# Kernel tuning notes

Measured on AMD Instinct MI355X. Metric: run time of the kernel, lower is better.

## Reference

```python
import jax, jax.numpy as jnp
import numpy as np

EPS = 1e-8
CG_TOL = 1e-4
S_SIGMA = 8   # bilateral grid spatial downsampling
N_BINS = 9    # bilateral grid range bins (intensity in [0,1])


def _conv2d(x, k):
    # x [C,H,W], k [kh,kw] -> same-padded cross-correlation, per channel
    kh, kw = k.shape
    out = jax.lax.conv_general_dilated(x[:, None], k[None, None], (1, 1),
                                       [(kh // 2, kh // 2), (kw // 2, kw // 2)])
    return out[:, 0]


def _conv2d_T(x, k):
    return _conv2d(x, k[::-1, ::-1])


def _conv_bank(x, ks):
    # x [C,H,W], ks [N,kh,kw] -> [N,C,H,W]
    n, kh, kw = ks.shape
    out = jax.lax.conv_general_dilated(x[:, None], ks[:, None], (1, 1),
                                       [(kh // 2, kh // 2), (kw // 2, kw // 2)])
    return out.transpose(1, 0, 2, 3)


def _conv_bank_T(v, ks):
    # v [N,C,H,W] -> sum_n conv(v[n], flip(ks[n])) : [C,H,W]
    n, kh, kw = ks.shape
    lhs = v.transpose(1, 0, 2, 3)          # [C,N,H,W]
    rhs = ks[:, ::-1, ::-1][None]          # [1,N,kh,kw]
    out = jax.lax.conv_general_dilated(lhs, rhs, (1, 1),
                                       [(kh // 2, kh // 2), (kw // 2, kw // 2)])
    return out[:, 0]


def _deconv_grad(blurred, x, kernel, dkw, dks, rkw, rks, rpow, reg_targets):
    # gradient of E(x) = sum_i dkw_i ||dk_i * (k*x - b)||^2
    #                  + sum_j rkw_j sum |rk_j*x - t_j|^{p_j}
    Kx = _conv2d(x, kernel) - blurred
    d = _conv_bank(Kx, dks)                                    # [Nd,C,H,W]
    g = _conv2d_T(_conv_bank_T(2.0 * dkw[:, None, None, None] * d, dks), kernel)
    v = _conv_bank(x, rks) - reg_targets                       # [Nr,C,H,W]
    av = jnp.abs(v) + EPS
    phi = jnp.sign(v) * av ** (rpow[:, None, None, None] - 1.0)
    g = g + _conv_bank_T(rkw[:, None, None, None] * rpow[:, None, None, None] * phi, rks)
    return g


def _deconv_alpha(blurred, x, kernel, dkw, dks, rkw, rks, rpow, reg_targets, p):
    # exact line search for the quadratic part, Gauss-Newton for |.|^p prior
    g = _deconv_grad(blurred, x, kernel, dkw, dks, rkw, rks, rpow, reg_targets)
    num = -jnp.sum(g * p)
    Kp = _conv2d(p, kernel)
    dKp = _conv_bank(Kp, dks)
    den = jnp.sum(2.0 * dkw[:, None, None, None] * dKp ** 2)
    v = _conv_bank(x, rks) - reg_targets
    Rp = _conv_bank(p, rks)
    w = (rkw * rpow * (rpow - 1.0))[:, None, None, None]
    den = den + jnp.sum(w * (jnp.abs(v) + EPS) ** (rpow[:, None, None, None] - 2.0) * Rp ** 2)
    return num / (den + 1e-12)


def _deconv_prior(x, rks, thr):
    # soft-shrinkage of filtered responses -> regularization targets
    v = _conv_bank(x, rks)
    return jnp.sign(v) * jnp.maximum(jnp.abs(v) - thr[:, None, None, None], 0.0)


def _conv_axis(g, f, axis):
    k = f.shape[0]; r = k // 2; L = g.shape[axis]
    pad = [(0, 0)] * g.ndim; pad[axis] = (r, r)
    gp = jnp.pad(g, pad)
    out = jnp.zeros_like(g)
    for t in range(k):  # fixed small tap count
        out = out + f[t] * jax.lax.slice_in_dim(gp, t, t + L, axis=axis)
    return out


def _bilateral_channel(I, fs, fr):
    # learned-filter bilateral grid: splat -> separable filter (fs,fs,fr) -> trilinear slice
    H, W = I.shape
    gh, gw = H // S_SIGMA, W // S_SIGMA
    Ic = jnp.clip(I, 0.0, 1.0)
    yy, xx = jnp.meshgrid(jnp.arange(H), jnp.arange(W), indexing="ij")
    yi = yy // S_SIGMA; xi = xx // S_SIGMA
    zi = jnp.clip(jnp.round(Ic * (N_BINS - 1)).astype(jnp.int32), 0, N_BINS - 1)
    flat = ((yi * gw + xi) * N_BINS + zi).ravel()
    gv = jnp.zeros(gh * gw * N_BINS, Ic.dtype).at[flat].add(Ic.ravel())
    gw_ = jnp.zeros(gh * gw * N_BINS, Ic.dtype).at[flat].add(1.0)
    g2 = jnp.stack([gv, gw_], -1).reshape(gh, gw, N_BINS, 2)
    g2 = _conv_axis(_conv_axis(_conv_axis(g2, fs, 0), fs, 1), fr, 2)
    yf = yy / S_SIGMA; xf = xx / S_SIGMA; zf = Ic * (N_BINS - 1)

    def corners(f, n):
        c0 = jnp.clip(jnp.floor(f).astype(jnp.int32), 0, n - 1)
        c1 = jnp.minimum(c0 + 1, n - 1)
        w = jnp.clip(f - c0, 0.0, 1.0)
        return c0, c1, w

    y0, y1, wy = corners(yf, gh)
    x0, x1, wx = corners(xf, gw)
    z0, z1, wz = corners(zf, N_BINS)
    acc = jnp.zeros(I.shape + (2,), Ic.dtype)
    for yc, wyc in ((y0, 1 - wy), (y1, wy)):
        for xc, wxc in ((x0, 1 - wx), (x1, wx)):
            for zc, wzc in ((z0, 1 - wz), (z1, wz)):
                acc = acc + (wyc * wxc * wzc)[..., None] * g2[yc, xc, zc]
    return acc[..., 0] / (acc[..., 1] + 1e-8)


def _forward(blurred_batch, kernel_batch, data_kernels, data_kernel_weights,
             reg_kernels, reg_kernel_weights, reg_powers, filter_s, filter_r,
             reg_thresholds, num_cg_iter):
    num_stages = filter_s.shape[0]
    n_reg = reg_kernels.shape[1]

    def single(blurred, kernel):
        def cg(x, idx, reg_targets):
            dkw = data_kernel_weights[idx]; dks = data_kernels[idx]
            rkw = reg_kernel_weights[idx]; rks = reg_kernels[idx]; rp = reg_powers[idx]
            g = _deconv_grad(blurred, x, kernel, dkw, dks, rkw, rks, rp, reg_targets)
            r = -g
            r_norm = jnp.sum(r * r)
            r0 = r_norm

            def body(i, carry):
                x, r, p, rn, done = carry
                alpha = _deconv_alpha(blurred, x, kernel, dkw, dks, rkw, rks, rp, reg_targets, p)
                x1 = x + alpha * p
                g1 = _deconv_grad(blurred, x1, kernel, dkw, dks, rkw, rks, rp, reg_targets)
                r1 = -g1
                nrn = jnp.sum(r1 * r1)
                beta = nrn / (rn + 1e-20)
                conv_now = nrn < CG_TOL * r0
                p1 = r1 + beta * p
                x_n = jnp.where(done, x, x1)
                r_n = jnp.where(done, r, r1)
                rn_n = jnp.where(done, rn, nrn)
                p_n = jnp.where(done | conv_now, p, p1)
                return (x_n, r_n, p_n, rn_n, done | conv_now)

            carry = (x, r, r, r_norm, jnp.array(False))
            x, _, _, _, _ = jax.lax.fori_loop(0, num_cg_iter, body, carry)
            return x

        x = cg(blurred, 0, jnp.zeros((n_reg,) + blurred.shape, blurred.dtype))
        for stage in range(num_stages):
            x = jax.vmap(lambda ch: _bilateral_channel(ch, filter_s[stage], filter_r[stage]))(x)
            reg_targets = _deconv_prior(x, reg_kernels[stage + 1], reg_thresholds[stage])
            x = cg(x, stage + 1, reg_targets)
        return x

    return jax.vmap(single)(blurred_batch, kernel_batch)


def setup_inputs() -> dict:
    key = jax.random.key(0)
    k1, k2 = jax.random.split(key)
    B, C, H, W, KS = 2, 3, 512, 512, 15
    blurred = jax.random.uniform(k1, (B, C, H, W), jnp.float32)
    kern = jax.random.uniform(k2, (B, KS, KS), jnp.float32)
    kern = kern / jnp.sum(kern, axis=(1, 2), keepdims=True)  # normalized PSFs

    ns = 1; c = 2  # num_stages, kernel center (5x5)
    rk = np.zeros((ns + 1, 5, 5, 5), np.float32)
    rk[:, 0, c, c] = -1.0; rk[:, 0, c + 1, c] = 1.0
    rk[:, 1, c, c] = -1.0; rk[:, 1, c, c + 1] = 1.0
    rk[:, 2, c, c] = 1.0; rk[:, 2, c + 1, c] = -1.0
    rk[:, 2, c, c + 1] = -1.0; rk[:, 2, c + 1, c + 1] = 1.0
    rk[:, 3, c - 1, c] = 1.0; rk[:, 3, c, c] = -2.0; rk[:, 3, c + 1, c] = 1.0
    rk[:, 4, c, c - 1] = 1.0; rk[:, 4, c, c] = -2.0; rk[:, 4, c, c + 1] = 1.0
    dk = np.zeros((ns + 1, 6, 5, 5), np.float32)
    dk[:, 0, c, c] = 1.0
    dk[:, 1:] = rk
    dkw = np.zeros((ns + 1, 6), np.float32); dkw[:, 0] = 1.0
    rkw = np.zeros((ns + 1, 5), np.float32)
    rkw[0, :] = 0.001; rkw[1:, :] = 0.05
    rpow = np.full((ns + 1, 5), 2.0, np.float32)
    fs = np.zeros((ns, 11), np.float32); fs[:, 3:8] = [0.0, 1.0, 2.0, 1.0, 0.0]
    fr = np.tile(np.array([0.0, 1.0, 2.0, 1.0, 0.0], np.float32), (ns, 1))
    thr = np.tile(np.array([0.065, 0.065, 0.0325, 0.0325, 0.0325], np.float32), (ns, 1))

    return {
        "blurred_batch": blurred,
        "kernel_batch": kern,
        "data_kernels": jnp.asarray(dk),
        "data_kernel_weights": jnp.asarray(dkw),
        "reg_kernels": jnp.asarray(rk),
        "reg_kernel_weights": jnp.asarray(rkw),
        "reg_powers": jnp.asarray(rpow),
        "filter_s": jnp.asarray(fs),
        "filter_r": jnp.asarray(fr),
        "reg_thresholds": jnp.asarray(thr),
        "num_cg_iter": 5,
    }


def reference(blurred_batch, kernel_batch, data_kernels, data_kernel_weights,
              reg_kernels, reg_kernel_weights, reg_powers, filter_s, filter_r,
              reg_thresholds, num_cg_iter):
    return _forward(blurred_batch, kernel_batch, data_kernels, data_kernel_weights,
                    reg_kernels, reg_kernel_weights, reg_powers, filter_s, filter_r,
                    reg_thresholds, num_cg_iter)
```

## Files before the change

### kernel.cpp

```cpp
#include <hip/hip_runtime.h>

constexpr int Bn = 2, Cn = 3, Hh = 512, Ww = 512;
constexpr int KS = 15, KR = 7;
constexpr int NDK = 6, NRK = 5;
constexpr int GH = 64, GW = 64, NBn = 9, SS = 8;
constexpr float EPSf = 1e-8f;
constexpr float CGTOL = 1e-4f;
constexpr int PLANE = Hh * Ww;
constexpr int CHW = Cn * PLANE;
constexpr int BX = 64, BY = 16;
constexpr int GXc = Ww / BX, GYc = Hh / BY;
constexpr int PB = GXc * GYc * Cn;
constexpr int SA = 80, THt = 30;
constexpr int S2W = 72, S2H = 24;
constexpr int PHW = 68, PHH = 20;
constexpr int PHG = (PHW / 4) * PHH;
constexpr int NITER = 5;

struct CgState { float alpha, beta, rn, r0; int done, pflag; int pad0, pad1; };

struct SolveInfo {
    int fastBank;
    int allrp2;
    int nd;
    int pad;
    float sctot;
    float dsc[NDK];
    int ddy[NDK], ddx[NDK];
    float C[81];
};

__device__ __forceinline__ float blockReduce(float v, float* red, int tid) {
    red[tid] = v; __syncthreads();
    for (int s = 128; s > 0; s >>= 1) { if (tid < s) red[tid] += red[tid + s]; __syncthreads(); }
    float r = red[0]; __syncthreads();
    return r;
}

__global__ __launch_bounds__(128)
void k_comp(const float* __restrict__ dkw, const float* __restrict__ dks,
            const float* __restrict__ rkw, const float* __restrict__ rpw,
            const float* __restrict__ rks, SolveInfo* si)
{
    const int idx = blockIdx.x;
    SolveInfo* s = si + idx;
    const float* dkw_i = dkw + idx * NDK;
    const float* dks_i = dks + (size_t)idx * NDK * 25;
    const float* rkw_i = rkw + idx * NRK;
    const float* rpw_i = rpw + idx * NRK;
    const float* rks_i = rks + (size_t)idx * NRK * 25;
    const int t = threadIdx.x;
    if (t < 81) {
        int oy = t / 9 - 4, ox = t % 9 - 4;
        float acc = 0.f;
        for (int m = 0; m < NRK; m++) {
            float wm = rkw_i[m], rp = rpw_i[m];
            float ch = wm * rp * (rp - 1.f);
            if (ch == 0.f) continue;
            for (int ay = 0; ay < 5; ay++)
                for (int ax = 0; ax < 5; ax++) {
                    int by = ay - oy, bx = ax - ox;
                    if (by < 0 || by >= 5 || bx < 0 || bx >= 5) continue;
                    acc += ch * rks_i[m * 25 + ay * 5 + ax] * rks_i[m * 25 + by * 5 + bx];
                }
        }
        s->C[t] = acc;
    }
    if (t == 81) {
        int fast = 1, nd = 0; float tot = 0.f;
        for (int n = 0; n < NDK; n++) {
            if (dkw_i[n] == 0.f) continue;
            int cntz = 0, pos = -1;
            for (int q = 0; q < 25; q++) if (dks_i[n * 25 + q] != 0.f) { cntz++; pos = q; }
            if (cntz > 1) fast = 0;
            if (cntz == 1 && nd < NDK) {
                float v = dks_i[n * 25 + pos];
                s->dsc[nd] = 2.f * dkw_i[n] * v * v;
                s->ddy[nd] = pos / 5 - 2; s->ddx[nd] = pos % 5 - 2;
                tot += s->dsc[nd]; nd++;
            }
        }
        s->fastBank = fast; s->nd = fast ? nd : 0; s->sctot = tot;
    }
    if (t == 82) {
        int ok = 1;
        for (int m = 0; m < NRK; m++) {
            float wm = rkw_i[m], rp = rpw_i[m];
            if (wm != 0.f && rp != 2.f && wm * rp * (rp - 1.f) != 0.f) ok = 0;
        }
        s->allrp2 = ok;
    }
}

__global__ __launch_bounds__(256)
void k_conv15(const float* __restrict__ src, const float* __restrict__ rb,
              const float* __restrict__ pbuf, float* __restrict__ aux2,
              const float* __restrict__ sub, float* __restrict__ out,
              const float* __restrict__ kernB, float* __restrict__ part,
              const SolveInfo* __restrict__ si,
              const CgState* __restrict__ st, const int* __restrict__ ncg,
              int iter, int mode)
{
    const int pz = blockIdx.z, b = pz / Cn, c = pz % Cn;
    const CgState s = st[b];
    if (mode == 2 && (s.done != 0 || iter >= *ncg)) return;
    __shared__ __align__(16) float tile[SA * THt];
    __shared__ float red[256];
    const int tx = threadIdx.x, ty = threadIdx.y, tid = ty * 16 + tx;
    const int ox0 = blockIdx.x * BX, oy0 = blockIdx.y * BY;
    const int baseP = pz * PLANE;
    const float beta = s.beta; const int pf = s.pflag;
// ... 88 lines not shown
    __shared__ __align__(16) float sl[S2W * S2H];
    __shared__ __align__(16) float dl[PHW * PHH];
    __shared__ float dkk[NDK * 25];
    __shared__ float dww[NDK];
    const int tx = threadIdx.x, ty = threadIdx.y, tid = ty * 16 + tx;
    const int ox0 = blockIdx.x * BX, oy0 = blockIdx.y * BY;
    const int baseP = pz * PLANE;
    const int colbase = tx * 4;
    for (int i = tid; i < NDK * 25; i += 256) dkk[i] = dks[i];
    if (tid < NDK) dww[tid] = dkw[tid];
    for (int i = tid; i < S2W * S2H; i += 256) {
        int ly = i / S2W, lx = i % S2W;
        int gy = oy0 - 4 + ly, gx = ox0 - 4 + lx;
        sl[i] = (gy >= 0 && gy < Hh && gx >= 0 && gx < Ww) ? sbuf[baseP + gy * Ww + gx] : 0.f;
    }
    __syncthreads();
    float t0 = 0.f, t1 = 0.f, t2 = 0.f, t3 = 0.f;
    for (int n = 0; n < NDK; n++) {
        float wn = 2.f * dww[n];
        if (wn == 0.f) continue;
        float dnr[25];
        #pragma unroll
        for (int q = 0; q < 25; q++) dnr[q] = dkk[n * 25 + q];
        for (int t = tid; t < PHG; t += 256) {
            int zy = t / 17, zx0 = (t % 17) * 4;
            int gy = oy0 - 2 + zy, gx0 = ox0 - 2 + zx0;
            float v0 = 0.f, v1 = 0.f, v2 = 0.f, v3 = 0.f;
            #pragma unroll
            for (int a = 0; a < 5; a++) {
                bool rz = dnr[a*5]==0.f && dnr[a*5+1]==0.f && dnr[a*5+2]==0.f &&
                          dnr[a*5+3]==0.f && dnr[a*5+4]==0.f;
                if (rz) continue;
                const float4* s4 = reinterpret_cast<const float4*>(&sl[(zy + a) * S2W + zx0]);
                float4 u0 = s4[0], u1 = s4[1];
                float f8[8] = {u0.x,u0.y,u0.z,u0.w,u1.x,u1.y,u1.z,u1.w};
                #pragma unroll
                for (int bb = 0; bb < 5; bb++) {
                    float kv = dnr[a * 5 + bb];
                    if (kv != 0.f) {
                        v0 = fmaf(kv, f8[bb], v0); v1 = fmaf(kv, f8[bb+1], v1);
                        v2 = fmaf(kv, f8[bb+2], v2); v3 = fmaf(kv, f8[bb+3], v3);
                    }
                }
            }
            bool gyin = (gy >= 0 && gy < Hh);
            if (!gyin || gx0     < 0 || gx0     >= Ww) v0 = 0.f;
            if (!gyin || gx0 + 1 < 0 || gx0 + 1 >= Ww) v1 = 0.f;
            if (!gyin || gx0 + 2 < 0 || gx0 + 2 >= Ww) v2 = 0.f;
            if (!gyin || gx0 + 3 < 0 || gx0 + 3 >= Ww) v3 = 0.f;
            *reinterpret_cast<float4*>(&dl[zy * PHW + zx0]) = make_float4(v0, v1, v2, v3);
        }
        __syncthreads();
        float c0 = 0.f, c1 = 0.f, c2 = 0.f, c3 = 0.f;
        #pragma unroll
        for (int a = 0; a < 5; a++) {
            int fr = 4 - a;
            bool rz = dnr[fr*5]==0.f && dnr[fr*5+1]==0.f && dnr[fr*5+2]==0.f &&
                      dnr[fr*5+3]==0.f && dnr[fr*5+4]==0.f;
            if (rz) continue;
            const float4* q4 = reinterpret_cast<const float4*>(&dl[(ty + a) * PHW + colbase]);
            float4 u0 = q4[0], u1 = q4[1];
            float f8[8] = {u0.x,u0.y,u0.z,u0.w,u1.x,u1.y,u1.z,u1.w};
            #pragma unroll
            for (int bb = 0; bb < 5; bb++) {
                float kv = dnr[fr * 5 + (4 - bb)];
                if (kv != 0.f) {
                    c0 = fmaf(kv, f8[bb], c0); c1 = fmaf(kv, f8[bb+1], c1);
                    c2 = fmaf(kv, f8[bb+2], c2); c3 = fmaf(kv, f8[bb+3], c3);
                }
            }
        }
        t0 = fmaf(wn, c0, t0); t1 = fmaf(wn, c1, t1);
        t2 = fmaf(wn, c2, t2); t3 = fmaf(wn, c3, t3);
        __syncthreads();
    }
    const int gi = baseP + (oy0 + ty) * Ww + ox0 + colbase;
    *reinterpret_cast<float4*>(&tbuf[gi]) = make_float4(t0, t1, t2, t3);
}

__global__ __launch_bounds__(256)
void k_hess(const float* __restrict__ kx, const float* __restrict__ wb,
            const float* __restrict__ pn,
            float* __restrict__ qb, const float* __restrict__ kernB,
            const float* __restrict__ rks, const float* __restrict__ rkw,
            const float* __restrict__ rpw, const SolveInfo* __restrict__ si,
            float* __restrict__ part, const CgState* __restrict__ st,
            const int* __restrict__ ncg, int iter)
{
    if (!si->allrp2) return;
    const int pz = blockIdx.z, b = pz / Cn, c = pz % Cn;
    const CgState s = st[b];
    if (s.done != 0 || iter >= *ncg) return;
    __shared__ __align__(16) float wt[SA * THt];
    __shared__ __align__(16) float s2[S2W * S2H];
    __shared__ __align__(16) float sC[81];
    __shared__ float rk5[NRK * 25];
    __shared__ float srkw[NRK], srpw[NRK];
    __shared__ float red[256];
    float* ph = wt;
    const int tx = threadIdx.x, ty = threadIdx.y, tid = ty * 16 + tx;
    const int ox0 = blockIdx.x * BX, oy0 = blockIdx.y * BY;
    const int baseP = pz * PLANE;
    const float* wsrc = si->fastBank ? kx : wb;
    const float* kp = kernB + b * 225;

    for (int i = tid; i < 81; i += 256) sC[i] = si->C[i];
    for (int i = tid; i < NRK * 25; i += 256) rk5[i] = rks[i];
    if (tid < NRK) { srkw[tid] = rkw[tid]; srpw[tid] = rpw[tid]; }

    for (int i = tid; i < 78 * THt; i += 256) {
        int ly = i / 78, lx = i % 78;
        int gy = oy0 - KR + ly, gx = ox0 - KR + lx;
        wt[ly * SA + lx] = (gy >= 0 && gy < Hh && gx >= 0 && gx < Ww)
                           ? wsrc[baseP + gy * Ww + gx] : 0.f;
    }
    for (int i = tid; i < S2W * S2H; i += 256) {
        int ly = i / S2W, lx = i % S2W;
        int gy = oy0 - 4 + ly, gx = ox0 - 4 + lx;
        s2[i] = (gy >= 0 && gy < Hh && gx >= 0 && gx < Ww)
                ? pn[baseP + gy * Ww + gx] : 0.f;
    }
    __syncthreads();

    const int colbase = tx * 4;
    float a0 = 0.f, a1 = 0.f, a2 = 0.f, a3 = 0.f;
    for (int i = 0; i < KS; i++) {
        const float4* rp4 = reinterpret_cast<const float4*>(&wt[(ty + i) * SA + colbase]);
        float f[20];
        #pragma unroll
        for (int s5 = 0; s5 < 5; s5++) {
            float4 w4 = rp4[s5];
            f[s5 * 4] = w4.x; f[s5 * 4 + 1] = w4.y; f[s5 * 4 + 2] = w4.z; f[s5 * 4 + 3] = w4.w;
        }
        const float* kr = kp + (14 - i) * 15;
        #pragma unroll
        for (int j = 0; j < KS; j++) {
            float kv = kr[14 - j];
            a0 = fmaf(kv, f[j], a0); a1 = fmaf(kv, f[j + 1], a1);
            a2 = fmaf(kv, f[j + 2], a2); a3 = fmaf(kv, f[j + 3], a3);
        }
    }

    const bool blkInterior = (oy0 >= 2) && (oy0 + BY - 1 <= Hh - 3) &&
                             (ox0 >= 2) && (ox0 + BX - 1 <= Ww - 3);
    if (blkInterior) {
        #pragma unroll
        for (int oy = 0; oy < 9; oy++) {
            float cr[9]; bool nz = false;
            #pragma unroll
            for (int ox = 0; ox < 9; ox++) { cr[ox] = sC[oy * 9 + ox]; nz = nz || (cr[ox] != 0.f); }
            if (!nz) continue;
            const float4* s4 = reinterpret_cast<const float4*>(&s2[(ty + oy) * S2W + colbase]);
            float4 u0 = s4[0], u1 = s4[1], u2 = s4[2];
            float f12[12] = {u0.x,u0.y,u0.z,u0.w,u1.x,u1.y,u1.z,u1.w,u2.x,u2.y,u2.z,u2.w};
            #pragma unroll
            for (int ox = 0; ox < 9; ox++) {
                float kv = cr[ox];
                if (kv != 0.f) {
                    a0 = fmaf(kv, f12[ox], a0); a1 = fmaf(kv, f12[ox + 1], a1);
                    a2 = fmaf(kv, f12[ox + 2], a2); a3 = fmaf(kv, f12[ox + 3], a3);
                }
            }
        }
    } else {
        __syncthreads();
        for (int m = 0; m < NRK; m++) {
            float wm = srkw[m], rp = srpw[m];
            float coefH = wm * rp * (rp - 1.f);
            if (coefH == 0.f) continue;
            float rmr[25];
            #pragma unroll
            for (int q = 0; q < 25; q++) rmr[q] = rk5[m * 25 + q];
            for (int t = tid; t < PHG; t += 256) {
                int zy = t / 17, zx0 = (t % 17) * 4;
                int gy = oy0 - 2 + zy, gx0 = ox0 - 2 + zx0;
                float v0 = 0.f, v1 = 0.f, v2 = 0.f, v3 = 0.f;
                #pragma unroll
                for (int a = 0; a < 5; a++) {
                    bool rz = rmr[a*5]==0.f && rmr[a*5+1]==0.f && rmr[a*5+2]==0.f &&
                              rmr[a*5+3]==0.f && rmr[a*5+4]==0.f;
                    if (rz) continue;
                    const float4* s4 = reinterpret_cast<const float4*>(&s2[(zy + a) * S2W + zx0]);
                    float4 u0 = s4[0], u1 = s4[1];
                    float f8[8] = {u0.x,u0.y,u0.z,u0.w,u1.x,u1.y,u1.z,u1.w};
                    #pragma unroll
                    for (int bb = 0; bb < 5; bb++) {
                        float kv = rmr[a * 5 + bb];
                        if (kv != 0.f) {
                            v0 = fmaf(kv, f8[bb], v0); v1 = fmaf(kv, f8[bb+1], v1);
                            v2 = fmaf(kv, f8[bb+2], v2); v3 = fmaf(kv, f8[bb+3], v3);
                        }
                    }
                }
                bool gyin = (gy >= 0 && gy < Hh);
                if (!gyin || gx0     < 0 || gx0     >= Ww) v0 = 0.f;
                if (!gyin || gx0 + 1 < 0 || gx0 + 1 >= Ww) v1 = 0.f;
                if (!gyin || gx0 + 2 < 0 || gx0 + 2 >= Ww) v2 = 0.f;
                if (!gyin || gx0 + 3 < 0 || gx0 + 3 >= Ww) v3 = 0.f;
                *reinterpret_cast<float4*>(&ph[zy * PHW + zx0]) =
                    make_float4(coefH * v0, coefH * v1, coefH * v2, coefH * v3);
            }
            __syncthreads();
            #pragma unroll
            for (int a = 0; a < 5; a++) {
                int fr = 4 - a;
                bool rz = rmr[fr*5]==0.f && rmr[fr*5+1]==0.f && rmr[fr*5+2]==0.f &&
                          rmr[fr*5+3]==0.f && rmr[fr*5+4]==0.f;
                if (rz) continue;
                const float4* q4 = reinterpret_cast<const float4*>(&ph[(ty + a) * PHW + colbase]);
                float4 u0 = q4[0], u1 = q4[1];
                float f8[8] = {u0.x,u0.y,u0.z,u0.w,u1.x,u1.y,u1.z,u1.w};
                #pragma unroll
                for (int bb = 0; bb < 5; bb++) {
                    float kv = rmr[fr * 5 + (4 - bb)];
                    if (kv != 0.f) {
                        a0 = fmaf(kv, f8[bb], a0); a1 = fmaf(kv, f8[bb+1], a1);
                        a2 = fmaf(kv, f8[bb+2], a2); a3 = fmaf(kv, f8[bb+3], a3);
                    }
                }
            }
            __syncthreads();
        }
    }

    const int gy = oy0 + ty, gx0 = ox0 + colbase;
    const int gi = baseP + gy * Ww + gx0;
    *reinterpret_cast<float4*>(&qb[gi]) = make_float4(a0, a1, a2, a3);
    int li = (ty + 4) * S2W + colbase + 4;
    float redv = s2[li] * a0 + s2[li + 1] * a1 + s2[li + 2] * a2 + s2[li + 3] * a3;
    float tot = blockReduce(redv, red, tid);
    if (tid == 0) {
        int blk = c * (GXc * GYc) + blockIdx.y * GXc + blockIdx.x;
        part[((size_t)b * 4 + 1) * PB + blk] = tot;
    }
}

__global__ __launch_bounds__(256)
void k_gradL(const float* __restrict__ kx, const float* __restrict__ wb,
             const float* __restrict__ xg,
             const float* __restrict__ rb, const float* __restrict__ pbuf,
             const float* __restrict__ tgt, const float* __restrict__ thr,
             float* __restrict__ outb,
             float* __restrict__ pout, const float* __restrict__ kernB,
             const float* __restrict__ rks, const float* __restrict__ rkw,
             const float* __restrict__ rpw, const SolveInfo* __restrict__ si,
             float* __restrict__ part, const CgState* __restrict__ st,
             const int* __restrict__ ncg, int iter, int mode)
{
    if (mode == 1 && si->allrp2) return;
    const int pz = blockIdx.z, b = pz / Cn, c = pz % Cn;
    const CgState s = st[b];
    if (mode == 1 && (s.done != 0 || iter >= *ncg)) return;
    __shared__ __align__(16) float wt[SA * THt];
    __shared__ __align__(16) float s2[S2W * S2H];
    __shared__ __align__(16) float sC[81];
    __shared__ float rk5[NRK * 25];
    __shared__ float srkw[NRK], srpw[NRK], sthr[NRK];
    __shared__ float red[256];
    float* ph = wt;
    const int tx = threadIdx.x, ty = threadIdx.y, tid = ty * 16 + tx;
    const int ox0 = blockIdx.x * BX, oy0 = blockIdx.y * BY;
    const int baseP = pz * PLANE;
    const float beta = s.beta; const int pf = s.pflag;
    const float* wsrc = si->fastBank ? kx : wb;
    const float* kp = kernB + b * 225;

    for (int i = tid; i < 81; i += 256) sC[i] = si->C[i];
    for (int i = tid; i < NRK * 25; i += 256) rk5[i] = rks[i];
    if (tid < NRK) {
        srkw[tid] = rkw[tid]; srpw[tid] = rpw[tid];
        sthr[tid] = thr ? thr[tid] : 0.f;
    }

    for (int i = tid; i < 78 * THt; i += 256) {
        int ly = i / 78, lx = i % 78;
        int gy = oy0 - KR + ly, gx = ox0 - KR + lx;
        wt[ly * SA + lx] = (gy >= 0 && gy < Hh && gx >= 0 && gx < Ww)
                           ? wsrc[baseP + gy * Ww + gx] : 0.f;
    }
    for (int i = tid; i < S2W * S2H; i += 256) {
        int ly = i / S2W, lx = i % S2W;
        int gy = oy0 - 4 + ly, gx = ox0 - 4 + lx;
        float v = 0.f;
        if (gy >= 0 && gy < Hh && gx >= 0 && gx < Ww) {
            int gi = baseP + gy * Ww + gx;
            if (mode == 0) v = xg[gi];
            else { float rv = rb[gi], pv = pbuf[gi]; v = pf ? fmaf(beta, pv, rv) : pv; }
        }
        s2[i] = v;
    }
    __syncthreads();

    const int colbase = tx * 4;
    float a0 = 0.f, a1 = 0.f, a2 = 0.f, a3 = 0.f;
    for (int i = 0; i < KS; i++) {
        const float4* rp4 = reinterpret_cast<const float4*>(&wt[(ty + i) * SA + colbase]);
        float f[20];
        #pragma unroll
        for (int s5 = 0; s5 < 5; s5++) {
            float4 w4 = rp4[s5];
            f[s5 * 4] = w4.x; f[s5 * 4 + 1] = w4.y; f[s5 * 4 + 2] = w4.z; f[s5 * 4 + 3] = w4.w;
        }
        const float* kr = kp + (14 - i) * 15;
        #pragma unroll
        for (int j = 0; j < KS; j++) {
            float kv = kr[14 - j];
            a0 = fmaf(kv, f[j], a0); a1 = fmaf(kv, f[j + 1], a1);
            a2 = fmaf(kv, f[j + 2], a2); a3 = fmaf(kv, f[j + 3], a3);
        }
    }

    const bool blkInterior = (oy0 >= 2) && (oy0 + BY - 1 <= Hh - 3) &&
                             (ox0 >= 2) && (ox0 + BX - 1 <= Ww - 3);
    if (mode == 0 && si->allrp2 && thr == nullptr && blkInterior) {
        #pragma unroll
        for (int oy = 0; oy < 9; oy++) {
            float cr[9]; bool nz = false;
            #pragma unroll
            for (int ox = 0; ox < 9; ox++) { cr[ox] = sC[oy * 9 + ox]; nz = nz || (cr[ox] != 0.f); }
            if (!nz) continue;
            const float4* s4 = reinterpret_cast<const float4*>(&s2[(ty + oy) * S2W + colbase]);
            float4 u0 = s4[0], u1 = s4[1], u2 = s4[2];
            float f12[12] = {u0.x,u0.y,u0.z,u0.w,u1.x,u1.y,u1.z,u1.w,u2.x,u2.y,u2.z,u2.w};
            #pragma unroll
            for (int ox = 0; ox < 9; ox++) {
                float kv = cr[ox];
                if (kv != 0.f) {
                    a0 = fmaf(kv, f12[ox], a0); a1 = fmaf(kv, f12[ox + 1], a1);
                    a2 = fmaf(kv, f12[ox + 2], a2); a3 = fmaf(kv, f12[ox + 3], a3);
                }
            }
        }
    } else {
        __syncthreads();
        for (int m = 0; m < NRK; m++) {
            float wm = srkw[m], rp = srpw[m];
            if (wm == 0.f) continue;
            float rmr[25];
            #pragma unroll
            for (int q = 0; q < 25; q++) rmr[q] = rk5[m * 25 + q];
            const float* tgm = (mode == 1 && tgt)
                ? tgt + ((size_t)(b * NRK + m)) * CHW + (size_t)c * PLANE : nullptr;
            const float coefG = wm * rp;
            const float coefH = wm * rp * (rp - 1.f);
            const float thrm = sthr[m];

            for (int t = tid; t < PHG; t += 256) {
                int zy = t / 17, zx0 = (t % 17) * 4;
                int gy = oy0 - 2 + zy, gx0 = ox0 - 2 + zx0;
                float v0 = 0.f, v1 = 0.f, v2 = 0.f, v3 = 0.f;
                #pragma unroll
                for (int a = 0; a < 5; a++) {
                    bool rz = rmr[a*5]==0.f && rmr[a*5+1]==0.f && rmr[a*5+2]==0.f &&
                              rmr[a*5+3]==0.f && rmr[a*5+4]==0.f;
                    if (rz) continue;
                    const float4* s4 = reinterpret_cast<const float4*>(&s2[(zy + a) * S2W + zx0]);
                    float4 u0 = s4[0], u1 = s4[1];
                    float f8[8] = {u0.x,u0.y,u0.z,u0.w,u1.x,u1.y,u1.z,u1.w};
                    #pragma unroll
                    for (int bb = 0; bb < 5; bb++) {
                        float kv = rmr[a * 5 + bb];
                        if (kv != 0.f) {
                            v0 = fmaf(kv, f8[bb], v0); v1 = fmaf(kv, f8[bb+1], v1);
                            v2 = fmaf(kv, f8[bb+2], v2); v3 = fmaf(kv, f8[bb+3], v3);
                        }
                    }
                }
                bool gyin = (gy >= 0 && gy < Hh);
                float o0 = 0.f, o1 = 0.f, o2 = 0.f, o3 = 0.f;
                #pragma unroll
                for (int j = 0; j < 4; j++) {
                    int gx = gx0 + j;
                    if (!gyin || gx < 0 || gx >= Ww) continue;
                    float v = (j == 0) ? v0 : (j == 1) ? v1 : (j == 2) ? v2 : v3;
                    float o;
                    if (mode == 0) {
                        if (thr) {
                            float sgv = (v > 0.f) ? 1.f : ((v < 0.f) ? -1.f : 0.f);
                            v = sgv * fminf(fabsf(v), thrm);
                        }
                        float sg = (v > 0.f) ? 1.f : ((v < 0.f) ? -1.f : 0.f);
                        float av = fabsf(v) + EPSf;
                        o = coefG * sg * ((rp == 2.f) ? av : powf(av, rp - 1.f));
                    } else {
                        float fac = 1.f;
                        if (rp != 2.f) {
                            float vx = 0.f;
                            for (int a = 0; a < 5; a++)
                                for (int bb = 0; bb < 5; bb++) {
                                    int yy = gy - 2 + a, xx = gx - 2 + bb;
                                    if (yy >= 0 && yy < Hh && xx >= 0 && xx < Ww)
                                        vx = fmaf(rmr[a * 5 + bb], xg[baseP + yy * Ww + xx], vx);
                                }
                            if (tgm) vx -= tgm[gy * Ww + gx];
                            fac = powf(fabsf(vx) + EPSf, rp - 2.f);
                        }
                        o = coefH * fac * v;
                    }
                    if (j == 0) o0 = o; else if (j == 1) o1 = o; else if (j == 2) o2 = o; else o3 = o;
                }
                *reinterpret_cast<float4*>(&ph[zy * PHW + zx0]) = make_float4(o0, o1, o2, o3);
            }
            __syncthreads();
            #pragma unroll
            for (int a = 0; a < 5; a++) {
                int fr = 4 - a;
                bool rz = rmr[fr*5]==0.f && rmr[fr*5+1]==0.f && rmr[fr*5+2]==0.f &&
                          rmr[fr*5+3]==0.f && rmr[fr*5+4]==0.f;
                if (rz) continue;
                const float4* q4 = reinterpret_cast<const float4*>(&ph[(ty + a) * PHW + colbase]);
                float4 u0 = q4[0], u1 = q4[1];
                float f8[8] = {u0.x,u0.y,u0.z,u0.w,u1.x,u1.y,u1.z,u1.w};
                #pragma unroll
                for (int bb = 0; bb < 5; bb++) {
                    float kv = rmr[fr * 5 + (4 - bb)];
                    if (kv != 0.f) {
                        a0 = fmaf(kv, f8[bb], a0); a1 = fmaf(kv, f8[bb+1], a1);
                        a2 = fmaf(kv, f8[bb+2], a2); a3 = fmaf(kv, f8[bb+3], a3);
                    }
                }
            }
            __syncthreads();
        }
    }

    const int gi = baseP + (oy0 + ty) * Ww + ox0 + colbase;
    float redv;
    if (mode == 0) {
        float r0v = -a0, r1v = -a1, r2v = -a2, r3v = -a3;
        float4 rv4 = make_float4(r0v, r1v, r2v, r3v);
        *reinterpret_cast<float4*>(&outb[gi]) = rv4;
        *reinterpret_cast<float4*>(&pout[gi]) = rv4;
        redv = r0v * r0v + r1v * r1v + r2v * r2v + r3v * r3v;
    } else {
        *reinterpret_cast<float4*>(&outb[gi]) = make_float4(a0, a1, a2, a3);
        int li = (ty + 4) * S2W + colbase + 4;
        redv = s2[li] * a0 + s2[li + 1] * a1 + s2[li + 2] * a2 + s2[li + 3] * a3;
    }
    float tot = blockReduce(redv, red, tid);
    if (tid == 0) {
        int blk = c * (GXc * GYc) + blockIdx.y * GXc + blockIdx.x;
        int slot = (mode == 0) ? 2 : 1;
        part[((size_t)b * 4 + slot) * PB + blk] = tot;
    }
}

__global__ __launch_bounds__(256)
void k_axpy(float4* __restrict__ x, float4* __restrict__ r,
            const float4* __restrict__ pn, const float4* __restrict__ q,
            float* __restrict__ part, const CgState* __restrict__ st,
            const int* __restrict__ ncg, int iter)
{
    const int b = blockIdx.y;
    const CgState s = st[b];
    if (s.done != 0 || iter >= *ncg) return;
    __shared__ float red[256];
    const int tid = threadIdx.x;
    float sn = 0.f, sd = 0.f;
    for (int i = tid; i < PB; i += 256) {
        sn += part[((size_t)b * 4 + 0) * PB + i];
        sd += part[((size_t)b * 4 + 1) * PB + i];
    }
    float num = blockReduce(sn, red, tid);
    float den = blockReduce(sd, red, tid);
    const float alpha = num / (den + 1e-12f);
    const int idx = b * (CHW / 4) + blockIdx.x * 256 + tid;
    float4 pc = pn[idx], rv = r[idx], qv = q[idx], xv = x[idx];
    xv.x = fmaf(alpha, pc.x, xv.x); xv.y = fmaf(alpha, pc.y, xv.y);
    xv.z = fmaf(alpha, pc.z, xv.z); xv.w = fmaf(alpha, pc.w, xv.w);
    rv.x = fmaf(-alpha, qv.x, rv.x); rv.y = fmaf(-alpha, qv.y, rv.y);
    rv.z = fmaf(-alpha, qv.z, rv.z); rv.w = fmaf(-alpha, qv.w, rv.w);
    x[idx] = xv; r[idx] = rv;
    float nr = rv.x * rv.x + rv.y * rv.y + rv.z * rv.z + rv.w * rv.w;
    float tot = blockReduce(nr, red, tid);
    if (tid == 0) part[((size_t)b * 4 + 2) * PB + blockIdx.x] = tot;
}

__global__ __launch_bounds__(256)
void k_fin_iter(const float* __restrict__ part, CgState* st,
                const int* __restrict__ ncg, int iter, int mode)
{
    const int b = blockIdx.x, tid = threadIdx.x;
    __shared__ float red[256];
    if (mode == 1 && (st[b].done != 0 || iter >= *ncg)) { if (tid == 0) st[b].pflag = 0; return; }
    float s = 0.f;
    for (int i = tid; i < PB; i += 256) s += part[((size_t)b * 4 + 2) * PB + i];
    float nrn = blockReduce(s, red, tid);
    if (tid == 0) {
        if (mode == 0) {
            st[b].rn = nrn; st[b].r0 = nrn; st[b].done = 0; st[b].pflag = 0;
            st[b].beta = 0.f; st[b].alpha = 0.f;
        } else {
            float beta = nrn / (st[b].rn + 1e-20f);
            int conv = (nrn < CGTOL * st[b].r0) ? 1 : 0;
            st[b].beta = beta; st[b].rn = nrn;
            st[b].pflag = conv ? 0 : 1;
            if (conv) st[b].done = 1;
        }
    }
}

__global__ __launch_bounds__(64)
void k_splat(const float* __restrict__ x, float* __restrict__ grid)
{
    __shared__ float bins[NBn * 2];
    const int tid = threadIdx.y * 8 + threadIdx.x;
    if (tid < NBn * 2) bins[tid] = 0.f;
    __syncthreads();
    const int pz = blockIdx.z;
    const int gy = blockIdx.y, gx = blockIdx.x;
    const int py = gy * 8 + threadIdx.y, px = gx * 8 + threadIdx.x;
    float I = x[(size_t)pz * PLANE + py * Ww + px];
    float Ic = fminf(fmaxf(I, 0.f), 1.f);
    int zi = (int)rintf(Ic * (NBn - 1));
    zi = min(max(zi, 0), NBn - 1);
    atomicAdd(&bins[zi * 2], Ic);
    atomicAdd(&bins[zi * 2 + 1], 1.f);
    __syncthreads();
    if (tid < NBn * 2)
        grid[(size_t)pz * GH * GW * NBn * 2 + ((size_t)gy * GW + gx) * NBn * 2 + tid] = bins[tid];
}

__global__ __launch_bounds__(256)
void k_blur(const float* __restrict__ in, float* __restrict__ out,
            const float* __restrict__ taps, int ntaps, int axis)
{
    const int id = blockIdx.x * 256 + threadIdx.x;
    const int total = Bn * Cn * GH * GW * NBn;
    if (id >= total) return;
    const int z = id % NBn;
    const int x = (id / NBn) % GW;
    const int y = (id / (NBn * GW)) % GH;
    const int p = id / (NBn * GW * GH);
    int coord, lim; long stride;
    if (axis == 0)      { coord = y; lim = GH;  stride = (long)GW * NBn * 2; }
    else if (axis == 1) { coord = x; lim = GW;  stride = NBn * 2; }
    else                { coord = z; lim = NBn; stride = 2; }
    const long base = (((long)(p * GH + y) * GW + x) * NBn + z) * 2;
    const int r = ntaps / 2;
    float a0 = 0.f, a1 = 0.f;
    for (int t = 0; t < ntaps; t++) {
        int cc = coord + t - r;
        if (cc < 0 || cc >= lim) continue;
        float w = taps[t];
        long ofs = base + (long)(cc - coord) * stride;
        a0 = fmaf(w, in[ofs], a0);
        a1 = fmaf(w, in[ofs + 1], a1);
    }
    out[base] = a0; out[base + 1] = a1;
}

__global__ __launch_bounds__(256)
void k_slice(const float* __restrict__ xin, const float* __restrict__ grid,
             float* __restrict__ xout)
{
    const int pz = blockIdx.z;
    const int id = blockIdx.x * 256 + threadIdx.x;
    const int py = id / Ww, px = id % Ww;
    float I = xin[(size_t)pz * PLANE + id];
    float Ic = fminf(fmaxf(I, 0.f), 1.f);
    float yf = (float)py / SS, xf = (float)px / SS, zf = Ic * (NBn - 1);
    int y0 = min(max((int)floorf(yf), 0), GH - 1); int y1 = min(y0 + 1, GH - 1);
    float wy = fminf(fmaxf(yf - (float)y0, 0.f), 1.f);
    int x0 = min(max((int)floorf(xf), 0), GW - 1); int x1 = min(x0 + 1, GW - 1);
    float wx = fminf(fmaxf(xf - (float)x0, 0.f), 1.f);
    int z0 = min(max((int)floorf(zf), 0), NBn - 1); int z1 = min(z0 + 1, NBn - 1);
    float wz = fminf(fmaxf(zf - (float)z0, 0.f), 1.f);
    const float* gp = grid + (size_t)pz * GH * GW * NBn * 2;
    const int   ys[2] = { y0, y1 };  const float wys[2] = { 1.f - wy, wy };
    const int   xs[2] = { x0, x1 };  const float wxs[2] = { 1.f - wx, wx };
    const int   zs[2] = { z0, z1 };  const float wzs[2] = { 1.f - wz, wz };
    float a0 = 0.f, a1 = 0.f;
    for (int iy = 0; iy < 2; iy++)
        for (int ix = 0; ix < 2; ix++)
            for (int iz = 0; iz < 2; iz++) {
                float w = wys[iy] * wxs[ix] * wzs[iz];
                size_t idx = (((size_t)ys[iy] * GW + xs[ix]) * NBn + zs[iz]) * 2;
                a0 = fmaf(w, gp[idx], a0);
                a1 = fmaf(w, gp[idx + 1], a1);
            }
    xout[(size_t)pz * PLANE + id] = a0 / (a1 + 1e-8f);
}

__global__ __launch_bounds__(256)
void k_prior(const float* __restrict__ x, float* __restrict__ tgt,
             const float* __restrict__ rks, const float* __restrict__ thr,
             const SolveInfo* __restrict__ si)
{
    if (si->allrp2) return;
    const int pz = blockIdx.z, b = pz / Cn, c = pz % Cn;
    __shared__ float xl[24 * 24];
    __shared__ float rkk[NRK * 25];
    __shared__ float sthr[NRK];
    const int tx = threadIdx.x, ty = threadIdx.y, tid = ty * 16 + tx;
    const int ox0 = blockIdx.x * 16, oy0 = blockIdx.y * 16;
    const int baseP = pz * PLANE;
    for (int i = tid; i < NRK * 25; i += 256) rkk[i] = rks[i];
    if (tid < NRK) sthr[tid] = thr[tid];
    for (int i = tid; i < 24 * 24; i += 256) {
        int ly = i / 24, lx = i % 24;
        int gy = oy0 - 2 + ly, gx = ox0 - 2 + lx;
        xl[i] = (gy >= 0 && gy < Hh && gx >= 0 && gx < Ww) ? x[baseP + gy * Ww + gx] : 0.f;
    }
    __syncthreads();
    const int pix = (oy0 + ty) * Ww + (ox0 + tx);
    for (int m = 0; m < NRK; m++) {
        const float* rm = &rkk[m * 25];
        float v = 0.f;
        #pragma unroll
        for (int a = 0; a < 5; a++)
            #pragma unroll
            for (int bb = 0; bb < 5; bb++)
                v = fmaf(rm[a * 5 + bb], xl[(ty + a) * 24 + (tx + bb)], v);
        float sg = (v > 0.f) ? 1.f : ((v < 0.f) ? -1.f : 0.f);
        tgt[((size_t)(b * NRK + m)) * CHW + (size_t)c * PLANE + pix] =
            sg * fmaxf(fabsf(v) - sthr[m], 0.f);
    }
}

extern "C" void kernel_launch(void* const* d_in, const int* in_sizes, int n_in,
                              void* d_out, int out_size, void* d_ws, size_t ws_size,
                              hipStream_t stream)
{
    const float* blurred = (const float*)d_in[0];
    const float* kern    = (const float*)d_in[1];
    const float* dks     = (const float*)d_in[2];
    const float* dkw     = (const float*)d_in[3];
    const float* rks     = (const float*)d_in[4];
    const float* rkw     = (const float*)d_in[5];
    const float* rpw     = (const float*)d_in[6];
    const float* fs      = (const float*)d_in[7];
    const float* fr      = (const float*)d_in[8];
    const float* thr     = (const float*)d_in[9];
    const int*   ncg     = (const int*)d_in[10];
    (void)in_sizes; (void)n_in; (void)out_size; (void)ws_size;

    float* w = (float*)d_ws;
    size_t off = 0;
    auto alloc = [&](size_t n) { float* p = w + off; off += n; return p; };
    float* xb    = alloc((size_t)Bn * CHW);
    float* pbufA = alloc((size_t)Bn * CHW);
    float* pbufB = alloc((size_t)Bn * CHW);
    float* rbuf  = alloc((size_t)Bn * CHW);
    float* kx    = alloc((size_t)Bn * CHW);
    float* wb    = alloc((size_t)Bn * CHW);
    float* qb    = alloc((size_t)Bn * CHW);
    float* tg    = alloc((size_t)Bn * NRK * CHW);
    float* g0    = alloc((size_t)Bn * Cn * GH * GW * NBn * 2);
    float* g1    = alloc((size_t)Bn * Cn * GH * GW * NBn * 2);
    float* part  = alloc((size_t)Bn * 4 * PB);
    CgState* st = (CgState*)(w + off); off += Bn * 8;
    SolveInfo* sinf = (SolveInfo*)(w + off); off += 2 * ((sizeof(SolveInfo) + 3) / 4);

    dim3 tb(16, 16), grd(GXc, GYc, Bn * Cn);

    k_comp<<<2, 128, 0, stream>>>(dkw, dks, rkw, rpw, rks, sinf);

    auto solve = [&](int idx, const float* tgt_i, const float* thr_i, int initmode) {
        const float* dks_i = dks + (size_t)idx * NDK * 25;
        const float* dkw_i = dkw + (size_t)idx * NDK;
        const float* rks_i = rks + (size_t)idx * NRK * 25;
        const float* rkw_i = rkw + (size_t)idx * NRK;
        const float* rpw_i = rpw + (size_t)idx * NRK;
        const SolveInfo* si = sinf + idx;
        k_conv15<<<grd, tb, 0, stream>>>(initmode == 0 ? blurred : xb, nullptr, nullptr,
                                         initmode == 0 ? xb : nullptr, blurred, kx, kern,
                                         nullptr, si, st, ncg, 0, initmode == 0 ? 0 : 3);
        k_bank<<<grd, tb, 0, stream>>>(kx, wb, dks_i, dkw_i, si, st, ncg, 0, 0);
        k_gradL<<<grd, tb, 0, stream>>>(kx, wb, xb, nullptr, nullptr, tgt_i, thr_i,
                                        rbuf, pbufA, kern,
                                        rks_i, rkw_i, rpw_i, si, part, st, ncg, 0, 0);
        k_fin_iter<<<Bn, 256, 0, stream>>>(part, st, ncg, 0, 0);
        float* pcur = pbufA;
        float* pnxt = pbufB;
        for (int i = 0; i < NITER; i++) {
            k_conv15<<<grd, tb, 0, stream>>>(nullptr, rbuf, pcur, pnxt, nullptr, kx, kern,
                                             part, si, st, ncg, i, 2);
            k_bank<<<grd, tb, 0, stream>>>(kx, wb, dks_i, dkw_i, si, st, ncg, i, 1);
            k_hess<<<grd, tb, 0, stream>>>(kx, wb, pnxt, qb, kern,
                                           rks_i, rkw_i, rpw_i, si, part, st, ncg, i);
            k_gradL<<<grd, tb, 0, stream>>>(kx, wb, xb, rbuf, pnxt, tgt_i, thr_i, qb, nullptr,
                                            kern, rks_i, rkw_i, rpw_i, si, part, st, ncg, i, 1);
            k_axpy<<<dim3(PB, Bn), 256, 0, stream>>>((float4*)xb, (float4*)rbuf,
                                                     (const float4*)pnxt, (const float4*)qb,
                                                     part, st, ncg, i);
            k_fin_iter<<<Bn, 256, 0, stream>>>(part, st, ncg, i, 1);
            float* tswap = pcur; pcur = pnxt; pnxt = tswap;
        }
    };

    solve(0, nullptr, nullptr, 0);

    dim3 sb(8, 8), sg(GW, GH, Bn * Cn);
    k_splat<<<sg, sb, 0, stream>>>(xb, g0);
    const int totalg = Bn * Cn * GH * GW * NBn;
    k_blur<<<(totalg + 255) / 256, 256, 0, stream>>>(g0, g1, fs, 11, 0);
    k_blur<<<(totalg + 255) / 256, 256, 0, stream>>>(g1, g0, fs, 11, 1);
    k_blur<<<(totalg + 255) / 256, 256, 0, stream>>>(g0, g1, fr, 5, 2);
    k_slice<<<dim3(PLANE / 256, 1, Bn * Cn), 256, 0, stream>>>(xb, g1, xb);

    k_prior<<<dim3(Ww / 16, Hh / 16, Bn * Cn), tb, 0, stream>>>(xb, tg, rks + NRK * 25, thr,
                                                                sinf + 1);

    solve(1, tg, thr, 1);

    hipMemcpyAsync(d_out, xb, (size_t)Bn * CHW * sizeof(float),
                   hipMemcpyDeviceToDevice, stream);
}
```

Baseline: 1.321 ms.

## Use stencil-only Hessian everywhere and correct image border with separate frame kernel

```diff
diff --git a/kernel.cpp b/kernel.cpp
--- a/kernel.cpp
+++ b/kernel.cpp
@@ -16,17 +16,16 @@
 constexpr int PHW = 68, PHH = 20;
 constexpr int PHG = (PHW / 4) * PHH;
 constexpr int NITER = 5;
+constexpr int FPP = 4080;
+constexpr int FBL = 17;
+constexpr int NFB = Cn * FBL;
 
 struct CgState { float alpha, beta, rn, r0; int done, pflag; int pad0, pad1; };
 
 struct SolveInfo {
-    int fastBank;
-    int allrp2;
-    int nd;
-    int pad;
+    int fastBank; int allrp2; int nd; int pad;
     float sctot;
-    float dsc[NDK];
-    int ddy[NDK], ddx[NDK];
+    float dsc[NDK]; int ddy[NDK], ddx[NDK];
     float C[81];
 };
 
@@ -281,8 +280,7 @@
 void k_hess(const float* __restrict__ kx, const float* __restrict__ wb,
             const float* __restrict__ pn,
             float* __restrict__ qb, const float* __restrict__ kernB,
-            const float* __restrict__ rks, const float* __restrict__ rkw,
-            const float* __restrict__ rpw, const SolveInfo* __restrict__ si,
+            const SolveInfo* __restrict__ si,
             float* __restrict__ part, const CgState* __restrict__ st,
             const int* __restrict__ ncg, int iter)
 {
@@ -293,10 +291,7 @@
     __shared__ __align__(16) float wt[SA * THt];
     __shared__ __align__(16) float s2[S2W * S2H];
     __shared__ __align__(16) float sC[81];
-    __shared__ float rk5[NRK * 25];
-    __shared__ float srkw[NRK], srpw[NRK];
     __shared__ float red[256];
-    float* ph = wt;
     const int tx = threadIdx.x, ty = threadIdx.y, tid = ty * 16 + tx;
     const int ox0 = blockIdx.x * BX, oy0 = blockIdx.y * BY;
     const int baseP = pz * PLANE;
@@ -304,8 +299,6 @@
     const float* kp = kernB + b * 225;
 
     for (int i = tid; i < 81; i += 256) sC[i] = si->C[i];
-    for (int i = tid; i < NRK * 25; i += 256) rk5[i] = rks[i];
-    if (tid < NRK) { srkw[tid] = rkw[tid]; srpw[tid] = rpw[tid]; }
 
     for (int i = tid; i < 78 * THt; i += 256) {
         int ly = i / 78, lx = i % 78;
@@ -340,85 +333,22 @@
         }
     }
 
-    const bool blkInterior = (oy0 >= 2) && (oy0 + BY - 1 <= Hh - 3) &&
-                             (ox0 >= 2) && (ox0 + BX - 1 <= Ww - 3);
-    if (blkInterior) {
-        #pragma unroll
-        for (int oy = 0; oy < 9; oy++) {
-            float cr[9]; bool nz = false;
-            #pragma unroll
-            for (int ox = 0; ox < 9; ox++) { cr[ox] = sC[oy * 9 + ox]; nz = nz || (cr[ox] != 0.f); }
-            if (!nz) continue;
-            const float4* s4 = reinterpret_cast<const float4*>(&s2[(ty + oy) * S2W + colbase]);
-            float4 u0 = s4[0], u1 = s4[1], u2 = s4[2];
-            float f12[12] = {u0.x,u0.y,u0.z,u0.w,u1.x,u1.y,u1.z,u1.w,u2.x,u2.y,u2.z,u2.w};
-            #pragma unroll
-            for (int ox = 0; ox < 9; ox++) {
-                float kv = cr[ox];
-                if (kv != 0.f) {
-                    a0 = fmaf(kv, f12[ox], a0); a1 = fmaf(kv, f12[ox + 1], a1);
-                    a2 = fmaf(kv, f12[ox + 2], a2); a3 = fmaf(kv, f12[ox + 3], a3);
-                }
-            }
-        }
-    } else {
-        __syncthreads();
-        for (int m = 0; m < NRK; m++) {
-            float wm = srkw[m], rp = srpw[m];
-            float coefH = wm * rp * (rp - 1.f);
-            if (coefH == 0.f) continue;
-            float rmr[25];
-            #pragma unroll
-            for (int q = 0; q < 25; q++) rmr[q] = rk5[m * 25 + q];
-            for (int t = tid; t < PHG; t += 256) {
-                int zy = t / 17, zx0 = (t % 17) * 4;
-                int gy = oy0 - 2 + zy, gx0 = ox0 - 2 + zx0;
-                float v0 = 0.f, v1 = 0.f, v2 = 0.f, v3 = 0.f;
-                #pragma unroll
-                for (int a = 0; a < 5; a++) {
-                    bool rz = rmr[a*5]==0.f && rmr[a*5+1]==0.f && rmr[a*5+2]==0.f &&
-                              rmr[a*5+3]==0.f && rmr[a*5+4]==0.f;
-                    if (rz) continue;
-                    const float4* s4 = reinterpret_cast<const float4*>(&s2[(zy + a) * S2W + zx0]);
-                    float4 u0 = s4[0], u1 = s4[1];
-                    float f8[8] = {u0.x,u0.y,u0.z,u0.w,u1.x,u1.y,u1.z,u1.w};
-                    #pragma unroll
-                    for (int bb = 0; bb < 5; bb++) {
-                        float kv = rmr[a * 5 + bb];
-                        if (kv != 0.f) {
-                            v0 = fmaf(kv, f8[bb], v0); v1 = fmaf(kv, f8[bb+1], v1);
-                            v2 = fmaf(kv, f8[bb+2], v2); v3 = fmaf(kv, f8[bb+3], v3);
-                        }
-                    }
-                }
-                bool gyin = (gy >= 0 && gy < Hh);
-                if (!gyin || gx0     < 0 || gx0     >= Ww) v0 = 0.f;
-                if (!gyin || gx0 + 1 < 0 || gx0 + 1 >= Ww) v1 = 0.f;
-                if (!gyin || gx0 + 2 < 0 || gx0 + 2 >= Ww) v2 = 0.f;
-                if (!gyin || gx0 + 3 < 0 || gx0 + 3 >= Ww) v3 = 0.f;
-                *reinterpret_cast<float4*>(&ph[zy * PHW + zx0]) =
-                    make_float4(coefH * v0, coefH * v1, coefH * v2, coefH * v3);
-            }
-            __syncthreads();
-            #pragma unroll
-            for (int a = 0; a < 5; a++) {
-                int fr = 4 - a;
-                bool rz = rmr[fr*5]==0.f && rmr[fr*5+1]==0.f && rmr[fr*5+2]==0.f &&
-                          rmr[fr*5+3]==0.f && rmr[fr*5+4]==0.f;
-                if (rz) continue;
-                const float4* q4 = reinterpret_cast<const float4*>(&ph[(ty + a) * PHW + colbase]);
-                float4 u0 = q4[0], u1 = q4[1];
-                float f8[8] = {u0.x,u0.y,u0.z,u0.w,u1.x,u1.y,u1.z,u1.w};
-                #pragma unroll
-                for (int bb = 0; bb < 5; bb++) {
-                    float kv = rmr[fr * 5 + (4 - bb)];
-                    if (kv != 0.f) {
-                        a0 = fmaf(kv, f8[bb], a0); a1 = fmaf(kv, f8[bb+1], a1);
-                        a2 = fmaf(kv, f8[bb+2], a2); a3 = fmaf(kv, f8[bb+3], a3);
-                    }
-                }
-            }
-            __syncthreads();
+    #pragma unroll
+    for (int oy = 0; oy < 9; oy++) {
+        float cr[9]; bool nz = false;
+        #pragma unroll
+        for (int ox = 0; ox < 9; ox++) { cr[ox] = sC[oy * 9 + ox]; nz = nz || (cr[ox] != 0.f); }
+        if (!nz) continue;
+        const float4* s4 = reinterpret_cast<const float4*>(&s2[(ty + oy) * S2W + colbase]);
+        float4 u0 = s4[0], u1 = s4[1], u2 = s4[2];
+        float f12[12] = {u0.x,u0.y,u0.z,u0.w,u1.x,u1.y,u1.z,u1.w,u2.x,u2.y,u2.z,u2.w};
+        #pragma unroll
+        for (int ox = 0; ox < 9; ox++) {
+            float kv = cr[ox];
+            if (kv != 0.f) {
+                a0 = fmaf(kv, f12[ox], a0); a1 = fmaf(kv, f12[ox + 1], a1);
+                a2 = fmaf(kv, f12[ox + 2], a2); a3 = fmaf(kv, f12[ox + 3], a3);
+            }
         }
     }
 
@@ -432,6 +362,72 @@
         int blk = c * (GXc * GYc) + blockIdx.y * GXc + blockIdx.x;
         part[((size_t)b * 4 + 1) * PB + blk] = tot;
     }
+}
+
+__global__ __launch_bounds__(256)
+void k_frame(const float* __restrict__ src,
+             float* __restrict__ tgtA,
+             float* __restrict__ tgtB,
+             const float* __restrict__ rks, const float* __restrict__ rkw,
+             const float* __restrict__ rpw, const SolveInfo* __restrict__ si,
+             float* __restrict__ part, const CgState* __restrict__ st,
+             const int* __restrict__ ncg, int iter, int mode)
+{
+    const int pz = blockIdx.y, b = pz / Cn;
+    if (mode == 1 && (st[b].done != 0 || iter >= *ncg)) return;
+    __shared__ float red[256];
+    const int tid = threadIdx.x;
+    const bool active = (si->allrp2 != 0);
+    const int fid = blockIdx.x * 256 + tid;
+    float contrib = 0.f;
+    if (active && fid < FPP) {
+        int gy, gx;
+        int r = fid;
+        if (r < 1024)       { gy = r >> 9;                 gx = r & 511; }
+        else if (r < 2048)  { gy = 510 + ((r - 1024) >> 9); gx = (r - 1024) & 511; }
+        else if (r < 3064)  { int q2 = r - 2048; gy = 2 + (q2 >> 1); gx = q2 & 1; }
+        else                { int q2 = r - 3064; gy = 2 + (q2 >> 1); gx = 510 + (q2 & 1); }
+        const float* sp = src + (size_t)pz * PLANE;
+        float corr = 0.f;
+        for (int ey = -2; ey <= 2; ey++) {
+            int zy = gy + ey;
+            for (int ex = -2; ex <= 2; ex++) {
+                int zx = gx + ex;
+                if (zy >= 0 && zy < Hh && zx >= 0 && zx < Ww) continue;
+                for (int m = 0; m < NRK; m++) {
+                    float cm = rkw[m] * rpw[m] * (rpw[m] - 1.f);
+                    if (cm == 0.f) continue;
+                    float tap = rks[m * 25 + (2 - ey) * 5 + (2 - ex)];
+                    if (tap == 0.f) continue;
+                    float d = 0.f;
+                    for (int a = 0; a < 5; a++)
+                        for (int bb = 0; bb < 5; bb++) {
+                            float kv = rks[m * 25 + a * 5 + bb];
+                            if (kv != 0.f) {
+                                int yy = zy - 2 + a, xx = zx - 2 + bb;
+                                if (yy >= 0 && yy < Hh && xx >= 0 && xx < Ww)
+                                    d = fmaf(kv, sp[yy * Ww + xx], d);
+                            }
+                        }
+                    corr = fmaf(cm * tap, d, corr);
+                }
+            }
+        }
+        const int gi = pz * PLANE + gy * Ww + gx;
+        if (mode == 0) {
+            float rv = tgtA[gi];
+            float rn2 = rv + corr;
+            tgtA[gi] = rn2; tgtB[gi] = rn2;
+            contrib = rn2 * rn2 - rv * rv;
+        } else {
+            float qv = tgtA[gi] - corr;
+            tgtA[gi] = qv;
+            contrib = sp[gy * Ww + gx] * corr;
+        }
+    }
+    float tot = blockReduce(contrib, red, tid);
+    if (tid == 0)
+        part[((size_t)b * 4 + 3) * PB + (pz % Cn) * FBL + blockIdx.x] = tot;
 }
 
 __global__ __launch_bounds__(256)
@@ -509,9 +505,7 @@
         }
     }
 
-    const bool blkInterior = (oy0 >= 2) && (oy0 + BY - 1 <= Hh - 3) &&
-                             (ox0 >= 2) && (ox0 + BX - 1 <= Ww - 3);
-    if (mode == 0 && si->allrp2 && thr == nullptr && blkInterior) {
+    if (mode == 0 && si->allrp2 && thr == nullptr) {
         #pragma unroll
         for (int oy = 0; oy < 9; oy++) {
             float cr[9]; bool nz = false;
@@ -660,6 +654,8 @@
         sn += part[((size_t)b * 4 + 0) * PB + i];
         sd += part[((size_t)b * 4 + 1) * PB + i];
     }
+    for (int i = tid; i < NFB; i += 256)
+        sd -= part[((size_t)b * 4 + 3) * PB + i];
     float num = blockReduce(sn, red, tid);
     float den = blockReduce(sd, red, tid);
     const float alpha = num / (den + 1e-12f);
@@ -677,13 +673,15 @@
 
 __global__ __launch_bounds__(256)
 void k_fin_iter(const float* __restrict__ part, CgState* st,
-                const int* __restrict__ ncg, int iter, int mode)
+                const int* __restrict__ ncg, int iter, int mode, int useExtra)
 {
     const int b = blockIdx.x, tid = threadIdx.x;
     __shared__ float red[256];
     if (mode == 1 && (st[b].done != 0 || iter >= *ncg)) { if (tid == 0) st[b].pflag = 0; return; }
     float s = 0.f;
     for (int i = tid; i < PB; i += 256) s += part[((size_t)b * 4 + 2) * PB + i];
+    if (mode == 0 && useExtra)
+        for (int i = tid; i < NFB; i += 256) s += part[((size_t)b * 4 + 3) * PB + i];
     float nrn = blockReduce(s, red, tid);
     if (tid == 0) {
         if (mode == 0) {
@@ -850,26 +848,33 @@
     float* part  = alloc((size_t)Bn * 4 * PB);
     CgState* st = (CgState*)(w + off); off += Bn * 8;
     SolveInfo* sinf = (SolveInfo*)(w + off); off += 2 * ((sizeof(SolveInfo) + 3) / 4);
+    float* xout = (float*)d_out;
 
     dim3 tb(16, 16), grd(GXc, GYc, Bn * Cn);
+    dim3 fgrd(FBL, Bn * Cn);
 
     k_comp<<<2, 128, 0, stream>>>(dkw, dks, rkw, rpw, rks, sinf);
 
-    auto solve = [&](int idx, const float* tgt_i, const float* thr_i, int initmode) {
+    auto solve = [&](int idx, float* xcur, const float* tgt_i, const float* thr_i,
+                     int initmode) {
         const float* dks_i = dks + (size_t)idx * NDK * 25;
         const float* dkw_i = dkw + (size_t)idx * NDK;
         const float* rks_i = rks + (size_t)idx * NRK * 25;
         const float* rkw_i = rkw + (size_t)idx * NRK;
         const float* rpw_i = rpw + (size_t)idx * NRK;
         const SolveInfo* si = sinf + idx;
-        k_conv15<<<grd, tb, 0, stream>>>(initmode == 0 ? blurred : xb, nullptr, nullptr,
-                                         initmode == 0 ? xb : nullptr, blurred, kx, kern,
+        k_conv15<<<grd, tb, 0, stream>>>(initmode == 0 ? blurred : xcur, nullptr, nullptr,
+                                         initmode == 0 ? xcur : nullptr, blurred, kx, kern,
                                          nullptr, si, st, ncg, 0, initmode == 0 ? 0 : 3);
         k_bank<<<grd, tb, 0, stream>>>(kx, wb, dks_i, dkw_i, si, st, ncg, 0, 0);
-        k_gradL<<<grd, tb, 0, stream>>>(kx, wb, xb, nullptr, nullptr, tgt_i, thr_i,
+        k_gradL<<<grd, tb, 0, stream>>>(kx, wb, xcur, nullptr, nullptr, tgt_i, thr_i,
                                         rbuf, pbufA, kern,
                                         rks_i, rkw_i, rpw_i, si, part, st, ncg, 0, 0);
-        k_fin_iter<<<Bn, 256, 0, stream>>>(part, st, ncg, 0, 0);
+        const int useFrame = (thr_i == nullptr) ? 1 : 0;
+        if (useFrame)
+            k_frame<<<fgrd, 256, 0, stream>>>(xcur, rbuf, pbufA, rks_i, rkw_i, rpw_i,
+                                              si, part, st, ncg, 0, 0);
+        k_fin_iter<<<Bn, 256, 0, stream>>>(part, st, ncg, 0, 0, useFrame);
         float* pcur = pbufA;
         float* pnxt = pbufB;
         for (int i = 0; i < NITER; i++) {
@@ -877,18 +882,20 @@
                                              part, si, st, ncg, i, 2);
             k_bank<<<grd, tb, 0, stream>>>(kx, wb, dks_i, dkw_i, si, st, ncg, i, 1);
             k_hess<<<grd, tb, 0, stream>>>(kx, wb, pnxt, qb, kern,
-                                           rks_i, rkw_i, rpw_i, si, part, st, ncg, i);
-            k_gradL<<<grd, tb, 0, stream>>>(kx, wb, xb, rbuf, pnxt, tgt_i, thr_i, qb, nullptr,
+                                           si, part, st, ncg, i);
+            k_frame<<<fgrd, 256, 0, stream>>>(pnxt, qb, nullptr, rks_i, rkw_i, rpw_i,
+                                              si, part, st, ncg, i, 1);
+            k_gradL<<<grd, tb, 0, stream>>>(kx, wb, xcur, rbuf, pnxt, tgt_i, thr_i, qb, nullptr,
                                             kern, rks_i, rkw_i, rpw_i, si, part, st, ncg, i, 1);
-            k_axpy<<<dim3(PB, Bn), 256, 0, stream>>>((float4*)xb, (float4*)rbuf,
+            k_axpy<<<dim3(PB, Bn), 256, 0, stream>>>((float4*)xcur, (float4*)rbuf,
                                                      (const float4*)pnxt, (const float4*)qb,
                                                      part, st, ncg, i);
-            k_fin_iter<<<Bn, 256, 0, stream>>>(part, st, ncg, i, 1);
+            k_fin_iter<<<Bn, 256, 0, stream>>>(part, st, ncg, i, 1, 0);
             float* tswap = pcur; pcur = pnxt; pnxt = tswap;
         }
     };
 
-    solve(0, nullptr, nullptr, 0);
+    solve(0, xb, nullptr, nullptr, 0);
 
     dim3 sb(8, 8), sg(GW, GH, Bn * Cn);
     k_splat<<<sg, sb, 0, stream>>>(xb, g0);
@@ -896,13 +903,10 @@
     k_blur<<<(totalg + 255) / 256, 256, 0, stream>>>(g0, g1, fs, 11, 0);
     k_blur<<<(totalg + 255) / 256, 256, 0, stream>>>(g1, g0, fs, 11, 1);
     k_blur<<<(totalg + 255) / 256, 256, 0, stream>>>(g0, g1, fr, 5, 2);
-    k_slice<<<dim3(PLANE / 256, 1, Bn * Cn), 256, 0, stream>>>(xb, g1, xb);
-
-    k_prior<<<dim3(Ww / 16, Hh / 16, Bn * Cn), tb, 0, stream>>>(xb, tg, rks + NRK * 25, thr,
+    k_slice<<<dim3(PLANE / 256, 1, Bn * Cn), 256, 0, stream>>>(xb, g1, xout);
+
+    k_prior<<<dim3(Ww / 16, Hh / 16, Bn * Cn), tb, 0, stream>>>(xout, tg, rks + NRK * 25, thr,
                                                                 sinf + 1);
 
-    solve(1, tg, thr, 1);
-
-    hipMemcpyAsync(d_out, xb, (size_t)Bn * CHW * sizeof(float),
-                   hipMemcpyDeviceToDevice, stream);
-}
+    solve(1, xout, tg, thr, 1);
+}
```

New measurement: 1.328 ms. About the same (+0.6%).
